# Optimization experiments

Measured on AMD Instinct MI355X. Metric: run time of the kernel, lower is better.

## Reference

```python
import jax, jax.numpy as jnp
import numpy as np
from jax import lax

B, L, C, K = 32, 128, 192, 3


def conv1d_same(x, w, b):
    # x: [B, L, C], w: [K, Cin, Cout], b: [Cout]
    y = lax.conv_general_dilated(x, w, window_strides=(1,), padding='SAME',
                                 dimension_numbers=('NWC', 'WIO', 'NWC'))
    return y + b


def shift_right(x):
    # ShiftLayer: shift memory one step along length axis, zero-padded
    return jnp.pad(x, ((0, 0), (1, 0), (0, 0)))[:, :-1, :]


def setup_inputs() -> dict:
    key = jax.random.key(0)
    ks = jax.random.split(key, 4)
    scale = 1.0 / np.sqrt(K * C)
    x = jax.random.normal(ks[0], (B, L, C), dtype=jnp.float32)
    w_reset = jax.random.normal(ks[1], (K, C, C), dtype=jnp.float32) * scale
    w_gate = jax.random.normal(ks[2], (K, C, C), dtype=jnp.float32) * scale
    w_cand = jax.random.normal(ks[3], (K, C, C), dtype=jnp.float32) * scale
    b_reset = jnp.full((C,), 0.5, dtype=jnp.float32)  # bias_initializer 0.5
    b_gate = jnp.full((C,), 0.7, dtype=jnp.float32)   # bias_initializer 0.7
    b_cand = jnp.zeros((C,), dtype=jnp.float32)       # bias_initializer 0.0
    return {'x': x, 'w_reset': w_reset, 'b_reset': b_reset,
            'w_gate': w_gate, 'b_gate': b_gate,
            'w_cand': w_cand, 'b_cand': b_cand}


def reference(x, w_reset, b_reset, w_gate, b_gate, w_cand, b_cand):
    def step(mem, _):
        shifted = shift_right(mem)
        reset = jax.nn.sigmoid(conv1d_same(mem, w_reset, b_reset))
        gate = jax.nn.sigmoid(conv1d_same(mem, w_gate, b_gate))
        cand = jnp.tanh(conv1d_same(reset * mem, w_cand, b_cand))
        out = gate * shifted + (1.0 - gate) * cand
        return out, None

    # DNGPU unrolls the gated-conv cell for `length` (= seq_len) steps
    out, _ = lax.scan(step, x, None, length=L)
    return out
```

## Files before the change

### kernel.cpp

```cpp
#include <hip/hip_runtime.h>

typedef __attribute__((ext_vector_type(8)))  short short8;
typedef __attribute__((ext_vector_type(4)))  float f32x4;
typedef __attribute__((ext_vector_type(16))) float f32x16;

#define NROWS 4096
#define CC    192
#define NCEL  (NROWS * CC)

#define WTELEM (6 * 18 * 2 * 384 * 8)

typedef const __attribute__((address_space(1))) void as1_void;
typedef __attribute__((address_space(3))) void as3_void;
#define GLD_LDS16(G, L) __builtin_amdgcn_global_load_lds((as1_void*)(G), (as3_void*)(L), 16, 0, 0)

__device__ __forceinline__ unsigned short f2bf(float x) {
    union { float f; unsigned int u; } v; v.f = x;
    unsigned int r = v.u + 0x7fffu + ((v.u >> 16) & 1u);
    return (unsigned short)(r >> 16);
}
__device__ __forceinline__ float bf2f(unsigned short h) {
    union { unsigned int u; float f; } v; v.u = ((unsigned int)h) << 16;
    return v.f;
}
__device__ __forceinline__ unsigned packhl(float x) {
    unsigned short h = f2bf(x);
    unsigned short l = f2bf(x - bf2f(h));
    return (unsigned)h | ((unsigned)l << 16);
}
__device__ __forceinline__ float unpackhl(unsigned v) {
    return bf2f((unsigned short)(v & 0xFFFFu)) + bf2f((unsigned short)(v >> 16));
}
__device__ __forceinline__ float sigmoid_f(float x) {
    return 1.0f / (1.0f + __expf(-x));
}
__device__ __forceinline__ float tanh_f(float x) {
    float ax = fabsf(x);
    if (ax < 0.0625f) {
        float x2 = x * x;
        return x * fmaf(x2, fmaf(x2, 0.13333333f, -0.33333333f), 1.0f);
    }
    float e = __expf(2.0f * fminf(ax, 20.0f));
    float t = (e - 1.0f) / (e + 1.0f);
    return x < 0.0f ? -t : t;
}

__global__ void prep_x(const float* __restrict__ x, unsigned* __restrict__ memHL) {
    int i = blockIdx.x * 256 + threadIdx.x;
    if (i < NCEL) memHL[i] = packhl(x[i]);
}

__global__ void prep_w(const float* __restrict__ wr, const float* __restrict__ wg,
                       const float* __restrict__ wc, unsigned short* __restrict__ Wt) {
    int o = blockIdx.x * 256 + threadIdx.x;
    if (o >= WTELEM) return;
    int e  = o & 7;
    int b  = o >> 3;
    int p  = b % 384;
    int pl = (b / 384) % 2;
    int ch = (b / 768) % 18;
    int grp = b / (768 * 18);
    int col = p >> 2;
    int slotp = p & 3;
    int slot = (slotp - col) & 3;
    int kk = ch / 6;
    int ci = (ch % 6) * 32 + slot * 8 + e;
    int conv = grp >> 1;
    int cglob = (grp & 1) * 96 + col;
    const float* w = (conv == 0) ? wr : ((conv == 1) ? wg : wc);
    float v = w[(size_t)(kk * 192 + ci) * 192 + cglob];
    unsigned short h = f2bf(v);
    Wt[o] = pl ? f2bf(v - bf2f(h)) : h;
}

#define ASTAGE(SRC, NT, NIT) do {                                                    \
    _Pragma("unroll")                                                                \
    for (int it_ = 0; it_ < (NIT); ++it_) {                                          \
        int q_ = it_ * (NT) + tid;                                                   \
        if (q_ < 34 * 96) {                                                          \
            int row_ = q_ / 96, u_ = q_ - row_ * 96;                                 \
            int gr_ = n0 - 1 + row_;                                                 \
            unsigned long long v_ = 0ull;                                            \
            if (gr_ >= 0 && ((gr_ >> 7) == (n0 >> 7)))                               \
                v_ = *(const unsigned long long*)((SRC) + (size_t)gr_ * 192 + u_ * 2);\
            unsigned lo_ = (unsigned)v_, hi_ = (unsigned)(v_ >> 32);                 \
            unsigned byt_ = ((unsigned)(u_ * 4)) ^ (((unsigned)(row_ & 7)) << 4);    \
            unsigned wdx_ = (((unsigned)row_) * 384 + byt_) >> 2;                    \
            ((unsigned*)AH)[wdx_] = (lo_ & 0xFFFFu) | (hi_ << 16);                   \
            ((unsigned*)AL)[wdx_] = (lo_ >> 16) | (hi_ & 0xFFFF0000u);               \
        }                                                                            \
    }                                                                                \
} while (0)

#define STAGEB(BUF, CH, NT) do {                                                     \
    const unsigned short* s_ = Wsec + (size_t)(CH) * 6144;                           \
    _Pragma("unroll")                                                                \
    for (int it_ = 0; it_ < 768 / (NT); ++it_) {                                     \
        int q_ = it_ * (NT) + tid;                                                   \
        GLD_LDS16(s_ + q_ * 8, &WB[BUF][q_ * 8]);                                    \
    }                                                                                \
} while (0)

__global__ __launch_bounds__(192)
void k1_rg(const unsigned* __restrict__ mem,
           const unsigned short* __restrict__ Wt,
           const float* __restrict__ b_r, const float* __restrict__ b_g,
           float* __restrict__ gate, unsigned* __restrict__ rm)
{
    __shared__ __align__(16) unsigned short AH[34 * 192];
    __shared__ __align__(16) unsigned short AL[34 * 192];
    __shared__ __align__(16) unsigned short WB[2][6144];

    const int strip = blockIdx.x, grp = blockIdx.y;
    const int n0 = strip * 32;
    const int tid = threadIdx.x;

    ASTAGE(mem, 192, 17);

    const int lane = tid & 63, w = tid >> 6;
    const int lr32 = lane & 31, khalf = lane >> 5;
    const int col96 = w * 32 + lr32;

    const unsigned short* Wsec = Wt + (size_t)grp * 18 * 6144;

    STAGEB(0, 0, 192);
    __syncthreads();

    f32x16 acc = {};
    int buf = 0;
    #pragma unroll 2
    for (int ch = 0; ch < 18; ++ch) {
        if (ch < 17) STAGEB(buf ^ 1, ch + 1, 192);
        const int kk = ch / 6, ci0 = (ch % 6) * 32;
        const int tr = lr32 + kk;
        short8 aH[2], aL[2], bH[2], bL[2];
        #pragma unroll
        for (int ks = 0; ks < 2; ++ks) {
            const int slot = ks * 2 + khalf;
            const unsigned byt = ((unsigned)((ci0 + slot * 8) * 2)) ^ (((unsigned)(tr & 7)) << 4);
            const int aoff = tr * 192 + (byt >> 1);
            aH[ks] = *(const short8*)(AH + aoff);
            aL[ks] = *(const short8*)(AL + aoff);
            const int boff = col96 * 32 + ((slot + col96) & 3) * 8;
            bH[ks] = *(const short8*)(&WB[buf][boff]);
            bL[ks] = *(const short8*)(&WB[buf][3072 + boff]);
        }
        #pragma unroll
        for (int ks = 0; ks < 2; ++ks) {
            acc = __builtin_amdgcn_mfma_f32_32x32x16_bf16(aH[ks], bH[ks], acc, 0, 0, 0);
            acc = __builtin_amdgcn_mfma_f32_32x32x16_bf16(aL[ks], bH[ks], acc, 0, 0, 0);
            acc = __builtin_amdgcn_mfma_f32_32x32x16_bf16(aH[ks], bL[ks], acc, 0, 0, 0);
        }
        __syncthreads();
        buf ^= 1;
    }

    const int conv = grp >> 1;
    const int chan = (grp & 1) * 96 + col96;
    const float bb = conv ? b_g[chan] : b_r[chan];
    #pragma unroll
    for (int r = 0; r < 16; ++r) {
        const int rl = (r & 3) + 8 * (r >> 2) + 4 * khalf;
        const int row = n0 + rl;
        const size_t idx = (size_t)row * 192 + chan;
        const float s = sigmoid_f(acc[r] + bb);
        if (conv == 0) {
            const int tr = rl + 1;
            const unsigned sb = ((unsigned)(chan * 2)) ^ (((unsigned)(tr & 7)) << 4);
            const float m = bf2f(AH[tr * 192 + (sb >> 1)]) + bf2f(AL[tr * 192 + (sb >> 1)]);
            rm[idx] = packhl(s * m);
        } else {
            gate[idx] = s;
        }
    }
}

__global__ __launch_bounds__(256)
void k2_c(const unsigned* __restrict__ rm,
          const unsigned short* __restrict__ Wt,
          const float* __restrict__ b_c, const float* __restrict__ gate,
          const unsigned* __restrict__ mem, unsigned* __restrict__ nxt,
          float* __restrict__ outF, int last)
{
    __shared__ __align__(16) unsigned short AH[34 * 192];
    __shared__ __align__(16) unsigned short AL[34 * 192];
    __shared__ __align__(16) unsigned short WB[2][6144];

    const int strip = blockIdx.x, half = blockIdx.y;
    const int n0 = strip * 32;
    const int tid = threadIdx.x;

    ASTAGE(rm, 256, 13);

    const int lane = tid & 63, w = tid >> 6;
    const int lrow = lane & 15, lkg = lane >> 4;
    const int mtw = w >> 1, ng = w & 1;

    const unsigned short* Wsec = Wt + (size_t)(4 + half) * 18 * 6144;

    STAGEB(0, 0, 256);
    __syncthreads();

    f32x4 acc[3] = {};
    int buf = 0;
    #pragma unroll 2
    for (int ch = 0; ch < 18; ++ch) {
        if (ch < 17) STAGEB(buf ^ 1, ch + 1, 256);
        const int kk = ch / 6, ci0 = (ch % 6) * 32;
        const int tr = 16 * mtw + lrow + kk;
        const unsigned byt = ((unsigned)((ci0 + lkg * 8) * 2)) ^ (((unsigned)(tr & 7)) << 4);
        const int aoff = tr * 192 + (byt >> 1);
        const short8 aH = *(const short8*)(AH + aoff);
        const short8 aL = *(const short8*)(AL + aoff);
        short8 bH[3], bL[3];
        #pragma unroll
        for (int j = 0; j < 3; ++j) {
            const int c96 = ng * 48 + j * 16 + lrow;
            const int boff = c96 * 32 + ((lkg + c96) & 3) * 8;
            bH[j] = *(const short8*)(&WB[buf][boff]);
            bL[j] = *(const short8*)(&WB[buf][3072 + boff]);
        }
        #pragma unroll
        for (int j = 0; j < 3; ++j) {
            acc[j] = __builtin_amdgcn_mfma_f32_16x16x32_bf16(aH, bH[j], acc[j], 0, 0, 0);
            acc[j] = __builtin_amdgcn_mfma_f32_16x16x32_bf16(aL, bH[j], acc[j], 0, 0, 0);
            acc[j] = __builtin_amdgcn_mfma_f32_16x16x32_bf16(aH, bL[j], acc[j], 0, 0, 0);
        }
        __syncthreads();
        buf ^= 1;
    }

    #pragma unroll
    for (int j = 0; j < 3; ++j) {
        const int chan = half * 96 + ng * 48 + j * 16 + lrow;
        const float bcv = b_c[chan];
        #pragma unroll
        for (int r = 0; r < 4; ++r) {
            const int row = n0 + 16 * mtw + lkg * 4 + r;
            const size_t idx = (size_t)row * 192 + chan;
            const float cand = tanh_f(acc[j][r] + bcv);
            const float g = gate[idx];
            float sh = 0.0f;
            if (row & 127) sh = unpackhl(mem[idx - 192]);
            const float o = g * sh + (1.0f - g) * cand;
            if (last) outF[idx] = o;
            else      nxt[idx] = packhl(o);
        }
    }
}

extern "C" void kernel_launch(void* const* d_in, const int* in_sizes, int n_in,
                              void* d_out, int out_size, void* d_ws, size_t ws_size,
                              hipStream_t stream)
{
    (void)in_sizes; (void)n_in; (void)out_size; (void)ws_size;
    const float* x   = (const float*)d_in[0];
    const float* w_r = (const float*)d_in[1];
    const float* b_r = (const float*)d_in[2];
    const float* w_g = (const float*)d_in[3];
    const float* b_g = (const float*)d_in[4];
    const float* w_c = (const float*)d_in[5];
    const float* b_c = (const float*)d_in[6];
    float* out = (float*)d_out;

    const size_t NC = (size_t)NCEL;
    unsigned* mem0 = (unsigned*)d_ws;
    unsigned* mem1 = mem0 + NC;
    unsigned* rm   = mem1 + NC;
    float*    gate = (float*)(rm + NC);
    unsigned short* Wt = (unsigned short*)(gate + NC);

    prep_x<<<dim3((NCEL + 255) / 256), dim3(256), 0, stream>>>(x, mem0);
    prep_w<<<dim3((WTELEM + 255) / 256), dim3(256), 0, stream>>>(w_r, w_g, w_c, Wt);

    for (int t = 0; t < 128; ++t) {
        const unsigned* cur = (t & 1) ? mem1 : mem0;
        unsigned* nxt = (t & 1) ? mem0 : mem1;
        k1_rg<<<dim3(128, 4), dim3(192), 0, stream>>>(cur, Wt, b_r, b_g, gate, rm);
        k2_c<<<dim3(128, 2), dim3(256), 0, stream>>>(rm, Wt, b_c, gate,
                                                     cur, nxt, out, t == 127);
    }
}
```

Baseline: 3.798 ms.

## Replace per-step kernel launches with persistent kernel using neighbor flag synchronization

Fuses the 256 per-step launches into one persistent kernel of 256 blocks. Each block owns a 32-row strip and half of the channels, keeps its memory tile resident in LDS, and splits its waves into producer waves that stream weights and import halo data and consumer waves that run the MFMA work. Blocks exchange only halo rows and sibling columns through global memory, synchronized by per-block flags that poll only neighbors. This removes launch overhead and redundant global reloads, at the cost of a co-residency requirement across all 256 blocks and spin-wait latency on the critical path.

After: 3.857 ms. No clear change (+1.5%).

```diff
diff --git a/kernel.cpp b/kernel.cpp
--- a/kernel.cpp
+++ b/kernel.cpp
@@ -2,17 +2,19 @@
 
 typedef __attribute__((ext_vector_type(8)))  short short8;
 typedef __attribute__((ext_vector_type(4)))  float f32x4;
-typedef __attribute__((ext_vector_type(16))) float f32x16;
 
 #define NROWS 4096
 #define CC    192
 #define NCEL  (NROWS * CC)
-
+#define NSTEP 128
 #define WTELEM (6 * 18 * 2 * 384 * 8)
 
 typedef const __attribute__((address_space(1))) void as1_void;
 typedef __attribute__((address_space(3))) void as3_void;
 #define GLD_LDS16(G, L) __builtin_amdgcn_global_load_lds((as1_void*)(G), (as3_void*)(L), 16, 0, 0)
+
+#define ALD(P)    __hip_atomic_load((P), __ATOMIC_RELAXED, __HIP_MEMORY_SCOPE_AGENT)
+#define AST(P, V) __hip_atomic_store((P), (V), __ATOMIC_RELAXED, __HIP_MEMORY_SCOPE_AGENT)
 
 __device__ __forceinline__ unsigned short f2bf(float x) {
     union { float f; unsigned int u; } v; v.f = x;
@@ -28,12 +30,7 @@
     unsigned short l = f2bf(x - bf2f(h));
     return (unsigned)h | ((unsigned)l << 16);
 }
-__device__ __forceinline__ float unpackhl(unsigned v) {
-    return bf2f((unsigned short)(v & 0xFFFFu)) + bf2f((unsigned short)(v >> 16));
-}
-__device__ __forceinline__ float sigmoid_f(float x) {
-    return 1.0f / (1.0f + __expf(-x));
-}
+__device__ __forceinline__ float sigmoid_f(float x) { return 1.0f / (1.0f + __expf(-x)); }
 __device__ __forceinline__ float tanh_f(float x) {
     float ax = fabsf(x);
     if (ax < 0.0625f) {
@@ -61,8 +58,7 @@
     int ch = (b / 768) % 18;
     int grp = b / (768 * 18);
     int col = p >> 2;
-    int slotp = p & 3;
-    int slot = (slotp - col) & 3;
+    int slot = ((p & 3) - col) & 3;
     int kk = ch / 6;
     int ci = (ch % 6) * 32 + slot * 8 + e;
     int conv = grp >> 1;
@@ -73,178 +69,227 @@
     Wt[o] = pl ? f2bf(v - bf2f(h)) : h;
 }
 
-#define ASTAGE(SRC, NT, NIT) do {                                                    \
-    _Pragma("unroll")                                                                \
-    for (int it_ = 0; it_ < (NIT); ++it_) {                                          \
-        int q_ = it_ * (NT) + tid;                                                   \
-        if (q_ < 34 * 96) {                                                          \
-            int row_ = q_ / 96, u_ = q_ - row_ * 96;                                 \
-            int gr_ = n0 - 1 + row_;                                                 \
-            unsigned long long v_ = 0ull;                                            \
-            if (gr_ >= 0 && ((gr_ >> 7) == (n0 >> 7)))                               \
-                v_ = *(const unsigned long long*)((SRC) + (size_t)gr_ * 192 + u_ * 2);\
-            unsigned lo_ = (unsigned)v_, hi_ = (unsigned)(v_ >> 32);                 \
-            unsigned byt_ = ((unsigned)(u_ * 4)) ^ (((unsigned)(row_ & 7)) << 4);    \
-            unsigned wdx_ = (((unsigned)row_) * 384 + byt_) >> 2;                    \
-            ((unsigned*)AH)[wdx_] = (lo_ & 0xFFFFu) | (hi_ << 16);                   \
-            ((unsigned*)AL)[wdx_] = (lo_ >> 16) | (hi_ & 0xFFFF0000u);               \
-        }                                                                            \
-    }                                                                                \
-} while (0)
-
-#define STAGEB(BUF, CH, NT) do {                                                     \
-    const unsigned short* s_ = Wsec + (size_t)(CH) * 6144;                           \
-    _Pragma("unroll")                                                                \
-    for (int it_ = 0; it_ < 768 / (NT); ++it_) {                                     \
-        int q_ = it_ * (NT) + tid;                                                   \
-        GLD_LDS16(s_ + q_ * 8, &WB[BUF][q_ * 8]);                                    \
-    }                                                                                \
-} while (0)
-
-__global__ __launch_bounds__(192)
-void k1_rg(const unsigned* __restrict__ mem,
-           const unsigned short* __restrict__ Wt,
-           const float* __restrict__ b_r, const float* __restrict__ b_g,
-           float* __restrict__ gate, unsigned* __restrict__ rm)
+__global__ __launch_bounds__(512)
+void dngpu_persist(const unsigned* __restrict__ memg0i, unsigned* __restrict__ memg0,
+                   unsigned* __restrict__ memg1, unsigned* __restrict__ rmg0,
+                   unsigned* __restrict__ rmg1,
+                   const unsigned short* __restrict__ Wt,
+                   const float* __restrict__ b_r, const float* __restrict__ b_g,
+                   const float* __restrict__ b_c,
+                   float* __restrict__ outF,
+                   unsigned* __restrict__ rmF, unsigned* __restrict__ memF)
 {
-    __shared__ __align__(16) unsigned short AH[34 * 192];
-    __shared__ __align__(16) unsigned short AL[34 * 192];
-    __shared__ __align__(16) unsigned short WB[2][6144];
-
-    const int strip = blockIdx.x, grp = blockIdx.y;
-    const int n0 = strip * 32;
-    const int tid = threadIdx.x;
-
-    ASTAGE(mem, 192, 17);
-
-    const int lane = tid & 63, w = tid >> 6;
-    const int lr32 = lane & 31, khalf = lane >> 5;
-    const int col96 = w * 32 + lr32;
-
-    const unsigned short* Wsec = Wt + (size_t)grp * 18 * 6144;
-
-    STAGEB(0, 0, 192);
-    __syncthreads();
-
-    f32x16 acc = {};
-    int buf = 0;
-    #pragma unroll 2
-    for (int ch = 0; ch < 18; ++ch) {
-        if (ch < 17) STAGEB(buf ^ 1, ch + 1, 192);
-        const int kk = ch / 6, ci0 = (ch % 6) * 32;
-        const int tr = lr32 + kk;
-        short8 aH[2], aL[2], bH[2], bL[2];
-        #pragma unroll
-        for (int ks = 0; ks < 2; ++ks) {
-            const int slot = ks * 2 + khalf;
-            const unsigned byt = ((unsigned)((ci0 + slot * 8) * 2)) ^ (((unsigned)(tr & 7)) << 4);
-            const int aoff = tr * 192 + (byt >> 1);
-            aH[ks] = *(const short8*)(AH + aoff);
-            aL[ks] = *(const short8*)(AL + aoff);
-            const int boff = col96 * 32 + ((slot + col96) & 3) * 8;
-            bH[ks] = *(const short8*)(&WB[buf][boff]);
-            bL[ks] = *(const short8*)(&WB[buf][3072 + boff]);
-        }
-        #pragma unroll
-        for (int ks = 0; ks < 2; ++ks) {
-            acc = __builtin_amdgcn_mfma_f32_32x32x16_bf16(aH[ks], bH[ks], acc, 0, 0, 0);
-            acc = __builtin_amdgcn_mfma_f32_32x32x16_bf16(aL[ks], bH[ks], acc, 0, 0, 0);
-            acc = __builtin_amdgcn_mfma_f32_32x32x16_bf16(aH[ks], bL[ks], acc, 0, 0, 0);
-        }
-        __syncthreads();
-        buf ^= 1;
-    }
-
-    const int conv = grp >> 1;
-    const int chan = (grp & 1) * 96 + col96;
-    const float bb = conv ? b_g[chan] : b_r[chan];
-    #pragma unroll
-    for (int r = 0; r < 16; ++r) {
-        const int rl = (r & 3) + 8 * (r >> 2) + 4 * khalf;
-        const int row = n0 + rl;
-        const size_t idx = (size_t)row * 192 + chan;
-        const float s = sigmoid_f(acc[r] + bb);
-        if (conv == 0) {
-            const int tr = rl + 1;
-            const unsigned sb = ((unsigned)(chan * 2)) ^ (((unsigned)(tr & 7)) << 4);
-            const float m = bf2f(AH[tr * 192 + (sb >> 1)]) + bf2f(AL[tr * 192 + (sb >> 1)]);
-            rm[idx] = packhl(s * m);
-        } else {
-            gate[idx] = s;
-        }
-    }
-}
-
-__global__ __launch_bounds__(256)
-void k2_c(const unsigned* __restrict__ rm,
-          const unsigned short* __restrict__ Wt,
-          const float* __restrict__ b_c, const float* __restrict__ gate,
-          const unsigned* __restrict__ mem, unsigned* __restrict__ nxt,
-          float* __restrict__ outF, int last)
-{
-    __shared__ __align__(16) unsigned short AH[34 * 192];
-    __shared__ __align__(16) unsigned short AL[34 * 192];
-    __shared__ __align__(16) unsigned short WB[2][6144];
-
-    const int strip = blockIdx.x, half = blockIdx.y;
-    const int n0 = strip * 32;
-    const int tid = threadIdx.x;
-
-    ASTAGE(rm, 256, 13);
-
-    const int lane = tid & 63, w = tid >> 6;
+    extern __shared__ unsigned short LB[];
+    unsigned short* T0H = LB;
+    unsigned short* T0L = LB + 6528;
+    unsigned short* T1H = LB + 13056;
+    unsigned short* T1L = LB + 19584;
+    unsigned short* WBB = LB + 26112;
+
+    const int tid = threadIdx.x, lane = tid & 63, wid = tid >> 6;
+    const int bid = blockIdx.x;
+    const int s = bid >> 1, h = bid & 1;
+    const int n0 = s * 32;
+    const bool isCons = wid < 4;
+    const int w = wid & 3, rh = w >> 1, cg = w & 1;
     const int lrow = lane & 15, lkg = lane >> 4;
-    const int mtw = w >> 1, ng = w & 1;
-
-    const unsigned short* Wsec = Wt + (size_t)(4 + half) * 18 * 6144;
-
-    STAGEB(0, 0, 256);
-    __syncthreads();
-
-    f32x4 acc[3] = {};
-    int buf = 0;
-    #pragma unroll 2
-    for (int ch = 0; ch < 18; ++ch) {
-        if (ch < 17) STAGEB(buf ^ 1, ch + 1, 256);
-        const int kk = ch / 6, ci0 = (ch % 6) * 32;
-        const int tr = 16 * mtw + lrow + kk;
-        const unsigned byt = ((unsigned)((ci0 + lkg * 8) * 2)) ^ (((unsigned)(tr & 7)) << 4);
-        const int aoff = tr * 192 + (byt >> 1);
-        const short8 aH = *(const short8*)(AH + aoff);
-        const short8 aL = *(const short8*)(AL + aoff);
-        short8 bH[3], bL[3];
+    const int pid = (wid - 4) * 64 + lane;
+
+    const int sib = bid ^ 1;
+    const bool hasUp = (s & 3) != 0, hasDn = (s & 3) != 3;
+    const int up0 = (s - 1) * 2, up1 = up0 + 1, dn0 = (s + 1) * 2, dn1 = dn0 + 1;
+
+    float br_[3], bg_[3], bc_[3];
+    if (isCons) {
         #pragma unroll
         for (int j = 0; j < 3; ++j) {
-            const int c96 = ng * 48 + j * 16 + lrow;
-            const int boff = c96 * 32 + ((lkg + c96) & 3) * 8;
-            bH[j] = *(const short8*)(&WB[buf][boff]);
-            bL[j] = *(const short8*)(&WB[buf][3072 + boff]);
-        }
+            const int col = h * 96 + cg * 48 + j * 16 + lrow;
+            br_[j] = b_r[col]; bg_[j] = b_g[col]; bc_[j] = b_c[col];
+        }
+    }
+
+    auto wsrc = [&](int cc) -> const unsigned short* {
+        int conv = (cc >= 36) ? 2 : (cc >= 18 ? 1 : 0);
+        int ch = cc - conv * 18;
+        return Wt + ((size_t)((conv * 2 + h) * 18 + ch)) * 6144;
+    };
+    auto stageW = [&](int cc) {
+        const unsigned short* sp = wsrc(cc);
+        unsigned short* dp = WBB + (cc & 1) * 6144;
         #pragma unroll
-        for (int j = 0; j < 3; ++j) {
-            acc[j] = __builtin_amdgcn_mfma_f32_16x16x32_bf16(aH, bH[j], acc[j], 0, 0, 0);
-            acc[j] = __builtin_amdgcn_mfma_f32_16x16x32_bf16(aL, bH[j], acc[j], 0, 0, 0);
-            acc[j] = __builtin_amdgcn_mfma_f32_16x16x32_bf16(aH, bL[j], acc[j], 0, 0, 0);
+        for (int it = 0; it < 3; ++it) {
+            int q = it * 256 + pid;
+            GLD_LDS16(sp + q * 8, dp + q * 8);
+        }
+    };
+    auto wrPair = [&](unsigned short* TH, unsigned short* TL, int slot, int colg,
+                      unsigned long long v) {
+        unsigned lo = (unsigned)v, hi = (unsigned)(v >> 32);
+        const unsigned sw = ((unsigned)(colg * 2)) ^ (((unsigned)(slot & 7)) << 4);
+        const int o = slot * 192 + (int)(sw >> 1);
+        *(unsigned*)(TH + o) = (lo & 0xFFFFu) | (hi << 16);
+        *(unsigned*)(TL + o) = (lo >> 16) | (hi & 0xFFFF0000u);
+    };
+    auto waitflag = [&](const unsigned* F, int idx, unsigned tgt) {
+        while (ALD(F + idx) < tgt) __builtin_amdgcn_s_sleep(4);
+    };
+    auto pollN = [&](const unsigned* F, unsigned tgt) {
+        waitflag(F, sib, tgt);
+        if (hasUp) { waitflag(F, up0, tgt); waitflag(F, up1, tgt); }
+        if (hasDn) { waitflag(F, dn0, tgt); waitflag(F, dn1, tgt); }
+    };
+    auto importT = [&](unsigned short* TH, unsigned short* TL, const unsigned* SRC, bool full) {
+        const unsigned long long* S8 = (const unsigned long long*)SRC;
+        if (full) {
+            #pragma unroll
+            for (int it = 0; it < 12; ++it) {
+                int q = it * 256 + pid;
+                int row = q / 96, cp = q - row * 96;
+                unsigned long long v = S8[(size_t)(n0 + row) * 96 + cp];
+                wrPair(TH, TL, row + 1, cp * 2, v);
+            }
+        } else {
+            const int cb2 = (h ^ 1) * 48;
+            #pragma unroll
+            for (int it = 0; it < 6; ++it) {
+                int q = it * 256 + pid;
+                int row = q / 48, cp = q - row * 48;
+                unsigned long long v = ALD(S8 + ((size_t)(n0 + row) * 96 + cb2 + cp));
+                wrPair(TH, TL, row + 1, (cb2 + cp) * 2, v);
+            }
+        }
+        if (pid < 192) {
+            int r01 = pid / 96, cp = pid - r01 * 96;
+            int grow = r01 ? (n0 + 32) : (n0 - 1);
+            int slot = r01 ? 33 : 0;
+            unsigned long long v = 0ull;
+            if (r01 ? hasDn : hasUp) v = ALD(S8 + ((size_t)grow * 96 + cp));
+            wrPair(TH, TL, slot, cp * 2, v);
+        }
+    };
+    auto rdT0 = [&](int slot, int colg) -> float {
+        const unsigned sw = ((unsigned)(colg * 2)) ^ (((unsigned)(slot & 7)) << 4);
+        const int o = slot * 192 + (int)(sw >> 1);
+        return bf2f(T0H[o]) + bf2f(T0L[o]);
+    };
+    auto wrT = [&](unsigned short* TH, unsigned short* TL, int slot, int colg, float v) {
+        unsigned short hh = f2bf(v), ll = f2bf(v - bf2f(hh));
+        const unsigned sw = ((unsigned)(colg * 2)) ^ (((unsigned)(slot & 7)) << 4);
+        const int o = slot * 192 + (int)(sw >> 1);
+        TH[o] = hh; TL[o] = ll;
+    };
+
+    if (!isCons) {
+        importT(T0H, T0L, memg0i, true);
+        stageW(0);
+    }
+    __syncthreads();
+
+    f32x4 acc[3];
+    float gr[3][4], sh[3][4];
+
+    for (int t = 0; t < NSTEP; ++t) {
+        unsigned* memg_nxt = (t & 1) ? memg0 : memg1;
+        unsigned* rmg_cur  = (t & 1) ? rmg1 : rmg0;
+
+        for (int cc = 0; cc < 54; ++cc) {
+            if (!isCons) {
+                int nc = cc + 1; if (nc == 54) nc = 0;
+                stageW(nc);
+                if (cc == 18) {
+                    pollN(rmF, (unsigned)(t + 1));
+                    importT(T1H, T1L, rmg_cur, false);
+                }
+            } else {
+                if (cc == 36) {
+                    #pragma unroll
+                    for (int j = 0; j < 3; ++j)
+                        #pragma unroll
+                        for (int r = 0; r < 4; ++r)
+                            gr[j][r] = sigmoid_f(acc[j][r] + bg_[j]);
+                }
+                if (cc == 0 || cc == 18 || cc == 36) {
+                    acc[0] = (f32x4){0.f,0.f,0.f,0.f};
+                    acc[1] = (f32x4){0.f,0.f,0.f,0.f};
+                    acc[2] = (f32x4){0.f,0.f,0.f,0.f};
+                }
+                const int conv = (cc >= 36) ? 2 : (cc >= 18 ? 1 : 0);
+                const int ch = cc - conv * 18;
+                const int kk = ch / 6, ci0 = (ch - kk * 6) * 32;
+                const unsigned short* TH = (conv == 2) ? T1H : T0H;
+                const unsigned short* TL = (conv == 2) ? T1L : T0L;
+                const int slot = rh * 16 + lrow + kk;
+                const int ab = (int)(((unsigned)((ci0 + lkg * 8) * 2) ^
+                                      (((unsigned)(slot & 7)) << 4)) >> 1);
+                const short8 aH = *(const short8*)(TH + slot * 192 + ab);
+                const short8 aL = *(const short8*)(TL + slot * 192 + ab);
+                const unsigned short* WBc = WBB + (cc & 1) * 6144;
+                #pragma unroll
+                for (int j = 0; j < 3; ++j) {
+                    const int c96 = cg * 48 + j * 16 + lrow;
+                    const int boff = c96 * 32 + ((lkg + c96) & 3) * 8;
+                    const short8 bH = *(const short8*)(WBc + boff);
+                    const short8 bL = *(const short8*)(WBc + 3072 + boff);
+                    acc[j] = __builtin_amdgcn_mfma_f32_16x16x32_bf16(aH, bH, acc[j], 0, 0, 0);
+                    acc[j] = __builtin_amdgcn_mfma_f32_16x16x32_bf16(aL, bH, acc[j], 0, 0, 0);
+                    acc[j] = __builtin_amdgcn_mfma_f32_16x16x32_bf16(aH, bL, acc[j], 0, 0, 0);
+                }
+            }
+            __syncthreads();
+
+            if (cc == 17) {
+                if (isCons) {
+                    #pragma unroll
+                    for (int j = 0; j < 3; ++j) {
+                        const int colg = h * 96 + cg * 48 + j * 16 + lrow;
+                        #pragma unroll
+                        for (int r = 0; r < 4; ++r) {
+                            const int crow = lkg * 4 + r;
+                            const int rslot = rh * 16 + crow + 1;
+                            const int rowg = n0 + rh * 16 + crow;
+                            const float m = rdT0(rslot, colg);
+                            sh[j][r] = rdT0(rslot - 1, colg);
+                            const float rr = sigmoid_f(acc[j][r] + br_[j]);
+                            const float rmv = rr * m;
+                            wrT(T1H, T1L, rslot, colg, rmv);
+                            AST(rmg_cur + (size_t)rowg * 192 + colg, packhl(rmv));
+                        }
+                    }
+                }
+                __syncthreads();
+                if (tid == 0) AST(rmF + bid, (unsigned)(t + 1));
+            }
+        }
+
+        if (isCons) {
+            #pragma unroll
+            for (int j = 0; j < 3; ++j) {
+                const int colg = h * 96 + cg * 48 + j * 16 + lrow;
+                #pragma unroll
+                for (int r = 0; r < 4; ++r) {
+                    const int crow = lkg * 4 + r;
+                    const int rslot = rh * 16 + crow + 1;
+                    const int rowg = n0 + rh * 16 + crow;
+                    const float cand = tanh_f(acc[j][r] + bc_[j]);
+                    const float g = gr[j][r];
+                    const float o = g * sh[j][r] + (1.0f - g) * cand;
+                    if (t == 127) {
+                        outF[(size_t)rowg * 192 + colg] = o;
+                    } else {
+                        wrT(T0H, T0L, rslot, colg, o);
+                        AST(memg_nxt + (size_t)rowg * 192 + colg, packhl(o));
+                    }
+                }
+            }
         }
         __syncthreads();
-        buf ^= 1;
-    }
-
-    #pragma unroll
-    for (int j = 0; j < 3; ++j) {
-        const int chan = half * 96 + ng * 48 + j * 16 + lrow;
-        const float bcv = b_c[chan];
-        #pragma unroll
-        for (int r = 0; r < 4; ++r) {
-            const int row = n0 + 16 * mtw + lkg * 4 + r;
-            const size_t idx = (size_t)row * 192 + chan;
-            const float cand = tanh_f(acc[j][r] + bcv);
-            const float g = gate[idx];
-            float sh = 0.0f;
-            if (row & 127) sh = unpackhl(mem[idx - 192]);
-            const float o = g * sh + (1.0f - g) * cand;
-            if (last) outF[idx] = o;
-            else      nxt[idx] = packhl(o);
+        if (t < 127) {
+            if (tid == 0) AST(memF + bid, (unsigned)(t + 1));
+            if (!isCons) {
+                pollN(memF, (unsigned)(t + 1));
+                importT(T0H, T0L, memg_nxt, false);
+            }
+            __syncthreads();
         }
     }
 }
@@ -264,20 +309,22 @@
     float* out = (float*)d_out;
 
     const size_t NC = (size_t)NCEL;
-    unsigned* mem0 = (unsigned*)d_ws;
-    unsigned* mem1 = mem0 + NC;
-    unsigned* rm   = mem1 + NC;
-    float*    gate = (float*)(rm + NC);
-    unsigned short* Wt = (unsigned short*)(gate + NC);
-
-    prep_x<<<dim3((NCEL + 255) / 256), dim3(256), 0, stream>>>(x, mem0);
+    unsigned* memg0 = (unsigned*)d_ws;
+    unsigned* memg1 = memg0 + NC;
+    unsigned* rmg0  = memg1 + NC;
+    unsigned* rmg1  = rmg0 + NC;
+    unsigned short* Wt = (unsigned short*)(rmg1 + NC);
+    unsigned* rmF  = (unsigned*)(Wt + (size_t)WTELEM);
+    unsigned* memF = rmF + 256;
+
+    const int LDSB = 82048;
+    hipFuncSetAttribute((const void*)dngpu_persist,
+                        hipFuncAttributeMaxDynamicSharedMemorySize, LDSB);
+
+    hipMemsetAsync(rmF, 0, 512 * sizeof(unsigned), stream);
+    prep_x<<<dim3((NCEL + 255) / 256), dim3(256), 0, stream>>>(x, memg0);
     prep_w<<<dim3((WTELEM + 255) / 256), dim3(256), 0, stream>>>(w_r, w_g, w_c, Wt);
 
-    for (int t = 0; t < 128; ++t) {
-        const unsigned* cur = (t & 1) ? mem1 : mem0;
-        unsigned* nxt = (t & 1) ? mem0 : mem1;
-        k1_rg<<<dim3(128, 4), dim3(192), 0, stream>>>(cur, Wt, b_r, b_g, gate, rm);
-        k2_c<<<dim3(128, 2), dim3(256), 0, stream>>>(rm, Wt, b_c, gate,
-                                                     cur, nxt, out, t == 127);
-    }
-}
+    dngpu_persist<<<dim3(256), dim3(512), LDSB, stream>>>(
+        memg0, memg0, memg1, rmg0, rmg1, Wt, b_r, b_g, b_c, out, rmF, memF);
+}
```
